# Kernel tuning notes

Measured on AMD Instinct MI355X. Metric: run time of the kernel, lower is better.

Reference implementation:

```python
import jax, jax.numpy as jnp
import numpy as np

NUM_REL = 20000
NUM_EDGES = 640000
DIM_IN = 128
DIM_OUT = 128
NUM_HEAD = 8
DIM_HID = DIM_OUT // NUM_HEAD
NUM_BIN = 10
NEG_SLOPE = 0.2


def leaky_relu(x):
    return jnp.where(x >= 0, x, NEG_SLOPE * x)


def setup_inputs() -> dict:
    key = jax.random.key(0)
    ks = jax.random.split(key, 8)
    emb_rel = jax.random.normal(ks[0], (NUM_REL, DIM_IN), dtype=jnp.float32)
    head = jax.random.randint(ks[1], (NUM_EDGES, 1), 0, NUM_REL)
    tail = jax.random.randint(ks[2], (NUM_EDGES, 1), 0, NUM_REL)
    bins = jax.random.randint(ks[3], (NUM_EDGES, 1), 0, NUM_BIN)
    relation_triplets = jnp.concatenate([head, tail, bins], axis=-1).astype(jnp.int64)
    # xavier-normal-ish init
    attn_proj_w = jax.random.normal(ks[4], (DIM_OUT, 2 * DIM_IN), dtype=jnp.float32) * (2.0 / np.sqrt(2 * DIM_IN + DIM_OUT))
    attn_proj_b = jnp.zeros((DIM_OUT,), dtype=jnp.float32)
    attn_bin = jax.random.normal(ks[5], (NUM_BIN, NUM_HEAD, 1), dtype=jnp.float32) * 0.3
    attn_vec = jax.random.normal(ks[6], (1, NUM_HEAD, DIM_HID), dtype=jnp.float32) * (2.0 / np.sqrt(NUM_HEAD * DIM_HID))
    aggr_proj_w = jax.random.normal(ks[7], (DIM_OUT, DIM_IN), dtype=jnp.float32) * (2.0 / np.sqrt(DIM_IN + DIM_OUT))
    aggr_proj_b = jnp.zeros((DIM_OUT,), dtype=jnp.float32)
    return {"emb_rel": emb_rel, "relation_triplets": relation_triplets,
            "attn_proj_w": attn_proj_w, "attn_proj_b": attn_proj_b,
            "attn_bin": attn_bin, "attn_vec": attn_vec,
            "aggr_proj_w": aggr_proj_w, "aggr_proj_b": aggr_proj_b}


def reference(emb_rel, relation_triplets, attn_proj_w, attn_proj_b, attn_bin, attn_vec, aggr_proj_w, aggr_proj_b):
    num_rel = emb_rel.shape[0]
    head = relation_triplets[..., 0]
    tail = relation_triplets[..., 1]
    bins = relation_triplets[..., 2]
    # edge gather + concat: [E, 2*dim_in]
    concat = jnp.concatenate([emb_rel[head], emb_rel[tail]], axis=-1)
    proj = concat @ attn_proj_w.T + attn_proj_b  # [E, dim_out]
    proj = leaky_relu(proj).reshape(-1, NUM_HEAD, DIM_HID)
    attn_raw = (proj * attn_vec).sum(axis=-1, keepdims=True) + leaky_relu(attn_bin[bins])  # [E,H,1]
    # per-head-relation segment softmax over edges grouped by head index
    seg_max = jax.ops.segment_max(attn_raw, head, num_segments=num_rel)  # [R,H,1]
    attn_val = jnp.exp(attn_raw - seg_max[head])
    seg_sum = jax.ops.segment_sum(attn_val, head, num_segments=num_rel)  # [R,H,1]
    beta = attn_val / (seg_sum[head] + 1e-16)
    msg = (emb_rel[tail] @ aggr_proj_w.T + aggr_proj_b).reshape(-1, NUM_HEAD, DIM_HID)
    out = jax.ops.segment_sum(beta * msg, head, num_segments=num_rel)  # [R,H,Dh]
    return out.reshape(num_rel, -1)
```

## Files before the change

### kernel.cpp

```cpp
#include <hip/hip_runtime.h>
#include <hip/hip_bf16.h>
#include <cstdint>
#include <cstddef>

#define NUM_REL    20000
#define NUM_EDGES  640000
#define DIM        128
#define NUM_HEAD   8
#define DIM_HID    16
#define NUM_BIN    10
#define CAP        128
#define PROJ_BLKS  471
#define SC_BLKS    2500

using u16 = unsigned short;
using u32 = unsigned int;
typedef __attribute__((ext_vector_type(8))) short bf16x8;
typedef __attribute__((ext_vector_type(4))) float f32x4;

__device__ __forceinline__ float b2f(u16 u) { return __uint_as_float(((u32)u) << 16); }
__device__ __forceinline__ float lo2f(u32 u) { return __uint_as_float(u << 16); }
__device__ __forceinline__ float hi2f(u32 u) { return __uint_as_float(u & 0xffff0000u); }
__device__ __forceinline__ float lrelu(float x) { return fmaxf(x, 0.2f * x); }
__device__ __forceinline__ int clampi(int v, int hi) { return v < 0 ? 0 : (v > hi ? hi : v); }
__device__ __forceinline__ float ldf(const void* p, int f32m, int i)
{ return f32m ? ((const float*)p)[i] : b2f(((const u16*)p)[i]); }
__device__ __forceinline__ u16 f2b(float x)
{ u32 u = __float_as_uint(x); u += 0x7fffu + ((u >> 16) & 1u); return (u16)(u >> 16); }
__device__ __forceinline__ u32 pk2(float a, float b)
{ return (u32)f2b(a) | ((u32)f2b(b) << 16); }

__global__ __launch_bounds__(256) void k_detect(
    const int* __restrict__ trip, const u16* __restrict__ emb,
    int* __restrict__ flags, int* __restrict__ cnt)
{
    int idx = blockIdx.x * 256 + threadIdx.x;
    if (idx < NUM_REL) cnt[idx] = 0;
    if (blockIdx.x == 0 && threadIdx.x < 64) {
        int t = threadIdx.x;
        bool odd_zero = (trip[2 * t + 1] == 0) && (trip[2 * t + 129] == 0);
        unsigned long long m1 = __ballot(odd_zero);
        int e = (emb[2 * t] >> 7) & 0xFF;
        bool inr = (e >= 110) && (e <= 136);
        unsigned long long m2 = __ballot(inr);
        if (t == 0) {
            flags[0] = (~m1 == 0ull) ? 1 : 0;
            flags[1] = (__popcll(m2) >= 32) ? 0 : 1;
        }
    }
}

__global__ __launch_bounds__(256) void k_projscatter(
    const void* __restrict__ emb, const int* __restrict__ trip,
    const void* __restrict__ w_attn, const void* __restrict__ w_aggr,
    const void* __restrict__ b_attn, const void* __restrict__ b_aggr,
    const int* __restrict__ flags,
    float* __restrict__ A, u16* __restrict__ Bb, u16* __restrict__ Mb,
    int* __restrict__ cnt, int* __restrict__ bucket)
{
    __shared__ u16 sA[128 * 128];
    __shared__ u16 sW[128 * 128];
    __shared__ float sBias[128];

    const int f32m = flags[1];
    const int tid = threadIdx.x;

    if (blockIdx.x >= PROJ_BLKS) {
        int e = (blockIdx.x - PROJ_BLKS) * 256 + tid;
        if (e < NUM_EDGES) {
            int h, t, b;
            if (flags[0]) { h = trip[6 * e]; t = trip[6 * e + 2]; b = trip[6 * e + 4]; }
            else          { h = trip[3 * e]; t = trip[3 * e + 1]; b = trip[3 * e + 2]; }
            h = clampi(h, NUM_REL - 1);
            t = clampi(t, NUM_REL - 1);
            b = clampi(b, NUM_BIN - 1);
            int pos = atomicAdd(&cnt[h], 1);
            if (pos < CAP) bucket[h * CAP + pos] = t | (b << 20);
        }
        return;
    }

    const int mt = blockIdx.x / 3, nt = blockIdx.x % 3;
    const int r0 = mt * 128;

    if (tid < 128)
        sBias[tid] = (nt == 0) ? 0.f : ldf((nt == 1) ? b_attn : b_aggr, f32m, tid);

    if (f32m) {
        const float* src = (const float*)emb;
        #pragma unroll
        for (int i = 0; i < 16; ++i) {
            int f = i * 256 + tid;
            int row = f >> 5, pos = f & 31;
            int g = r0 + row;
            float4 x = (g < NUM_REL) ? ((const float4*)(src + (size_t)g * DIM))[pos]
                                     : make_float4(0.f, 0.f, 0.f, 0.f);
            int chunk = (pos >> 1) ^ (row & 15);
            *(uint2*)&sA[row * 128 + chunk * 8 + (pos & 1) * 4] =
                make_uint2(pk2(x.x, x.y), pk2(x.z, x.w));
        }
    } else {
        const u16* src = (const u16*)emb;
        #pragma unroll
        for (int i = 0; i < 8; ++i) {
            int f = i * 256 + tid;
            int row = f >> 4, pos = f & 15;
            int g = r0 + row;
            uint4 x = (g < NUM_REL) ? ((const uint4*)(src + (size_t)g * DIM))[pos]
                                    : make_uint4(0, 0, 0, 0);
            int chunk = pos ^ (row & 15);
            *(uint4*)&sA[row * 128 + chunk * 8] = x;
        }
    }

    {
        const void* wsrc = (nt == 2) ? w_aggr : w_attn;
        const int stride = (nt == 2) ? 128 : 256;
        const int koff   = (nt == 1) ? 128 : 0;
        if (f32m) {
            const float* src = (const float*)wsrc;
            #pragma unroll
            for (int i = 0; i < 16; ++i) {
                int f = i * 256 + tid;
                int row = f >> 5, pos = f & 31;
                float4 x = ((const float4*)(src + (size_t)row * stride + koff))[pos];
                int chunk = (pos >> 1) ^ (row & 15);
                *(uint2*)&sW[row * 128 + chunk * 8 + (pos & 1) * 4] =
                    make_uint2(pk2(x.x, x.y), pk2(x.z, x.w));
            }
        } else {
            const u16* src = (const u16*)wsrc;
            #pragma unroll
            for (int i = 0; i < 8; ++i) {
                int f = i * 256 + tid;
                int row = f >> 4, pos = f & 15;
                uint4 x = ((const uint4*)(src + (size_t)row * stride + koff))[pos];
                int chunk = pos ^ (row & 15);
                *(uint4*)&sW[row * 128 + chunk * 8] = x;
            }
        }
    }
    __syncthreads();

    const int lane = tid & 63, wid = tid >> 6;
    const int wm = (wid >> 1) * 64, wn = (wid & 1) * 64;
    const int ln15 = lane & 15, q = lane >> 4;

    f32x4 acc[4][4] = {};
    #pragma unroll
    for (int kk = 0; kk < 4; ++kk) {
        const int cbase = kk * 4 + q;
        bf16x8 a[4], b[4];
        #pragma unroll
        for (int mi = 0; mi < 4; ++mi) {
            int m = wm + mi * 16 + ln15;
            int c = cbase ^ ln15;
            a[mi] = *(const bf16x8*)&sA[m * 128 + c * 8];
        }
        #pragma unroll
        for (int ni = 0; ni < 4; ++ni) {
            int n = wn + ni * 16 + ln15;
            int c = cbase ^ ln15;
            b[ni] = *(const bf16x8*)&sW[n * 128 + c * 8];
        }
        #pragma unroll
        for (int mi = 0; mi < 4; ++mi)
            #pragma unroll
            for (int ni = 0; ni < 4; ++ni)
                acc[mi][ni] = __builtin_amdgcn_mfma_f32_16x16x32_bf16(
                    a[mi], b[ni], acc[mi][ni], 0, 0, 0);
    }

    #pragma unroll
    for (int mi = 0; mi < 4; ++mi) {
        #pragma unroll
        for (int reg = 0; reg < 4; ++reg) {
            int g = r0 + wm + mi * 16 + q * 4 + reg;
            if (g < NUM_REL) {
                #pragma unroll
                for (int ni = 0; ni < 4; ++ni) {
                    int c = wn + ni * 16 + ln15;
                    float v = acc[mi][ni][reg] + sBias[c];
                    size_t o = (size_t)g * DIM + c;
                    if (nt == 0)      A[o]  = v;
                    else if (nt == 1) Bb[o] = f2b(v);
                    else              Mb[o] = f2b(v);
                }
            }
        }
    }
}

__global__ __launch_bounds__(256, 6) void k_segment(
    const float* __restrict__ A, const u16* __restrict__ Bb,
    const u16* __restrict__ Mb, const void* __restrict__ attn_bin,
    const void* __restrict__ attn_vec, const int* __restrict__ cnt,
    const int* __restrict__ bucket, const int* __restrict__ flags,
    void* __restrict__ out)
{
    __shared__ float sAr[4][DIM];
    __shared__ float sVec[DIM];
    __shared__ float sBin[NUM_BIN * NUM_HEAD];

    const int f32m = flags[1];
    const int tid  = threadIdx.x;
    const int wid  = tid >> 6, lane = tid & 63;
    const int r = blockIdx.x * 4 + wid;
    int nE = cnt[r]; if (nE > CAP) nE = CAP;
    const int* __restrict__ bk = bucket + r * CAP;

    {
        const float2* ap = (const float2*)(A + (size_t)r * DIM);
        float2 a2 = ap[lane];
        sAr[wid][2 * lane] = a2.x; sAr[wid][2 * lane + 1] = a2.y;
    }
    if (tid < DIM) sVec[tid] = ldf(attn_vec, f32m, tid);
    else if (tid < DIM + NUM_BIN * NUM_HEAD)
        sBin[tid - DIM] = lrelu(ldf(attn_bin, f32m, tid - DIM));
    __syncthreads();

    if (nE == 0) {
        if (f32m) ((float2*)out)[(size_t)r * 64 + lane] = make_float2(0.f, 0.f);
        else      ((u32*)out)[(size_t)r * 64 + lane] = 0;
        return;
    }

    const int el = lane >> 3, hd = lane & 7;
    const int ah = lane >> 3;

    float av[16], vv[16];
    {
        const float4* pA = (const float4*)(&sAr[wid][hd * DIM_HID]);
        const float4* pV = (const float4*)(&sVec[hd * DIM_HID]);
        #pragma unroll
        for (int i = 0; i < 4; ++i) {
            float4 a4 = pA[i], v4 = pV[i];
            av[4*i+0]=a4.x; av[4*i+1]=a4.y; av[4*i+2]=a4.z; av[4*i+3]=a4.w;
            vv[4*i+0]=v4.x; vv[4*i+1]=v4.y; vv[4*i+2]=v4.z; vv[4*i+3]=v4.w;
        }
    }

    float l = 0.f, accx = 0.f, accy = 0.f;

    for (int base = 0; base < nE; base += 8) {
        int e = base + el;
        bool act = e < nE;
        int tb = 0;
        if (act) tb = bk[e];
        int t = tb & 0xFFFFF;
        float p = 0.f;
        if (act) {
            int b = (tb >> 20) & 0xF;
            const uint4* Bt = (const uint4*)(Bb + (size_t)t * DIM) + hd * 2;
            uint4 q0 = Bt[0], q1 = Bt[1];
            float s = sBin[b * NUM_HEAD + hd];
            s += lrelu(av[0]  + lo2f(q0.x)) * vv[0];
            s += lrelu(av[1]  + hi2f(q0.x)) * vv[1];
            s += lrelu(av[2]  + lo2f(q0.y)) * vv[2];
            s += lrelu(av[3]  + hi2f(q0.y)) * vv[3];
            s += lrelu(av[4]  + lo2f(q0.z)) * vv[4];
            s += lrelu(av[5]  + hi2f(q0.z)) * vv[5];
            s += lrelu(av[6]  + lo2f(q0.w)) * vv[6];
            s += lrelu(av[7]  + hi2f(q0.w)) * vv[7];
            s += lrelu(av[8]  + lo2f(q1.x)) * vv[8];
            s += lrelu(av[9]  + hi2f(q1.x)) * vv[9];
            s += lrelu(av[10] + lo2f(q1.y)) * vv[10];
            s += lrelu(av[11] + hi2f(q1.y)) * vv[11];
            s += lrelu(av[12] + lo2f(q1.z)) * vv[12];
            s += lrelu(av[13] + hi2f(q1.z)) * vv[13];
            s += lrelu(av[14] + lo2f(q1.w)) * vv[14];
            s += lrelu(av[15] + hi2f(q1.w)) * vv[15];
            s = fminf(fmaxf(s, -60.f), 60.f);
            p = __expf(s);
        }
        l += p;

        int lim = nE - base; if (lim > 8) lim = 8;
        #pragma unroll
        for (int k = 0; k < 8; ++k) {
            if (k < lim) {
                float v = __shfl(p, k * 8 + ah);
                int tk  = __shfl(t, k * 8);
                u32 mm = *(const u32*)(Mb + (size_t)tk * DIM + 2 * lane);
                accx += v * lo2f(mm);
                accy += v * hi2f(mm);
            }
        }
    }

    float lt = l + __shfl_xor(l, 8);
    lt += __shfl_xor(lt, 16);
    lt += __shfl_xor(lt, 32);
    float lA = __shfl(lt, ah);
    float inv = 1.0f / (lA + 1e-16f);
    float o0 = accx * inv, o1 = accy * inv;
    if (f32m) {
        ((float2*)out)[(size_t)r * 64 + lane] = make_float2(o0, o1);
    } else {
        u32 pk = (u32)f2b(o0) | ((u32)f2b(o1) << 16);
        ((u32*)out)[(size_t)r * 64 + lane] = pk;
    }
}

extern "C" void kernel_launch(void* const* d_in, const int* in_sizes, int n_in,
                              void* d_out, int out_size, void* d_ws, size_t ws_size,
                              hipStream_t stream)
{
    (void)in_sizes; (void)n_in; (void)out_size; (void)ws_size;
    const void* emb      = d_in[0];
    const int*  trip     = (const int*)d_in[1];
    const void* w_attn   = d_in[2];
    const void* b_attn   = d_in[3];
    const void* attn_bin = d_in[4];
    const void* attn_vec = d_in[5];
    const void* w_aggr   = d_in[6];
    const void* b_aggr   = d_in[7];

    char* p = (char*)d_ws;
    float* A      = (float*)p; p += (size_t)NUM_REL * DIM * 4;
    u16*   Bb     = (u16*)p;   p += (size_t)NUM_REL * DIM * 2;
    u16*   Mb     = (u16*)p;   p += (size_t)NUM_REL * DIM * 2;
    int*   bucket = (int*)p;   p += (size_t)NUM_REL * CAP * 4;
    int*   cnt    = (int*)p;   p += (size_t)NUM_REL * 4;
    int*   flags  = (int*)p;   p += 256;

    k_detect<<<80, 256, 0, stream>>>(trip, (const u16*)emb, flags, cnt);
    k_projscatter<<<PROJ_BLKS + SC_BLKS, 256, 0, stream>>>(
        emb, trip, w_attn, w_aggr, b_attn, b_aggr, flags, A, Bb, Mb, cnt, bucket);
    k_segment<<<NUM_REL / 4, 256, 0, stream>>>(A, Bb, Mb, attn_bin, attn_vec,
                                               cnt, bucket, flags, d_out);
}
```

Measured before the change: 189.6 us.

## Inline format detection per block and software-prefetch next edge batch in segment loop

Removes the separate detect kernel: each block now recomputes the format flags in shared memory, and the count array is zeroed with a memset. In the segment kernel, the bucket entry and Bb row for the next group of 8 edges are loaded before computing the current group, so gather latency overlaps with compute. The cost is redundant flag detection in every block, an extra __syncthreads, higher register pressure from the prefetched values, and always-issued loads for inactive edges (these fall back to row 0).

```diff
diff --git a/kernel.cpp b/kernel.cpp
--- a/kernel.cpp
+++ b/kernel.cpp
@@ -30,47 +30,46 @@
 __device__ __forceinline__ u32 pk2(float a, float b)
 { return (u32)f2b(a) | ((u32)f2b(b) << 16); }
 
-__global__ __launch_bounds__(256) void k_detect(
-    const int* __restrict__ trip, const u16* __restrict__ emb,
-    int* __restrict__ flags, int* __restrict__ cnt)
+__device__ __forceinline__ void detect_flags(const int* __restrict__ trip,
+                                             const u16* __restrict__ emb,
+                                             int* sF, int tid)
 {
-    int idx = blockIdx.x * 256 + threadIdx.x;
-    if (idx < NUM_REL) cnt[idx] = 0;
-    if (blockIdx.x == 0 && threadIdx.x < 64) {
-        int t = threadIdx.x;
-        bool odd_zero = (trip[2 * t + 1] == 0) && (trip[2 * t + 129] == 0);
+    if (tid < 64) {
+        bool odd_zero = (trip[2 * tid + 1] == 0) && (trip[2 * tid + 129] == 0);
         unsigned long long m1 = __ballot(odd_zero);
-        int e = (emb[2 * t] >> 7) & 0xFF;
-        bool inr = (e >= 110) && (e <= 136);
+        int ex = (emb[2 * tid] >> 7) & 0xFF;
+        bool inr = (ex >= 110) && (ex <= 136);
         unsigned long long m2 = __ballot(inr);
-        if (t == 0) {
-            flags[0] = (~m1 == 0ull) ? 1 : 0;
-            flags[1] = (__popcll(m2) >= 32) ? 0 : 1;
-        }
-    }
+        if (tid == 0) {
+            sF[0] = (~m1 == 0ull) ? 1 : 0;
+            sF[1] = (__popcll(m2) >= 32) ? 0 : 1;
+        }
+    }
+    __syncthreads();
 }
 
 __global__ __launch_bounds__(256) void k_projscatter(
     const void* __restrict__ emb, const int* __restrict__ trip,
     const void* __restrict__ w_attn, const void* __restrict__ w_aggr,
     const void* __restrict__ b_attn, const void* __restrict__ b_aggr,
-    const int* __restrict__ flags,
     float* __restrict__ A, u16* __restrict__ Bb, u16* __restrict__ Mb,
     int* __restrict__ cnt, int* __restrict__ bucket)
 {
     __shared__ u16 sA[128 * 128];
     __shared__ u16 sW[128 * 128];
     __shared__ float sBias[128];
-
-    const int f32m = flags[1];
+    __shared__ int sF[2];
+
     const int tid = threadIdx.x;
+    detect_flags(trip, (const u16*)emb, sF, tid);
+    const int is64 = sF[0], f32m = sF[1];
 
     if (blockIdx.x >= PROJ_BLKS) {
         int e = (blockIdx.x - PROJ_BLKS) * 256 + tid;
         if (e < NUM_EDGES) {
             int h, t, b;
-            if (flags[0]) { h = trip[6 * e]; t = trip[6 * e + 2]; b = trip[6 * e + 4]; }
-            else          { h = trip[3 * e]; t = trip[3 * e + 1]; b = trip[3 * e + 2]; }
+            if (is64) { h = trip[6 * e]; t = trip[6 * e + 2]; b = trip[6 * e + 4]; }
+            else      { h = trip[3 * e]; t = trip[3 * e + 1]; b = trip[3 * e + 2]; }
             h = clampi(h, NUM_REL - 1);
             t = clampi(t, NUM_REL - 1);
             b = clampi(b, NUM_BIN - 1);
@@ -195,15 +194,18 @@
     const float* __restrict__ A, const u16* __restrict__ Bb,
     const u16* __restrict__ Mb, const void* __restrict__ attn_bin,
     const void* __restrict__ attn_vec, const int* __restrict__ cnt,
-    const int* __restrict__ bucket, const int* __restrict__ flags,
-    void* __restrict__ out)
+    const int* __restrict__ bucket, const int* __restrict__ trip,
+    const void* __restrict__ emb, void* __restrict__ out)
 {
     __shared__ float sAr[4][DIM];
     __shared__ float sVec[DIM];
     __shared__ float sBin[NUM_BIN * NUM_HEAD];
-
-    const int f32m = flags[1];
+    __shared__ int sF[2];
+
     const int tid  = threadIdx.x;
+    detect_flags(trip, (const u16*)emb, sF, tid);
+    const int f32m = sF[1];
+
     const int wid  = tid >> 6, lane = tid & 63;
     const int r = blockIdx.x * 4 + wid;
     int nE = cnt[r]; if (nE > CAP) nE = CAP;
@@ -242,17 +244,23 @@
 
     float l = 0.f, accx = 0.f, accy = 0.f;
 
+    bool act = el < nE;
+    int tb = act ? bk[el] : 0;
+    int t  = tb & 0xFFFFF;
+    const uint4* Bt0p = (const uint4*)(Bb + (size_t)t * DIM) + hd * 2;
+    uint4 q0 = Bt0p[0], q1 = Bt0p[1];
+
     for (int base = 0; base < nE; base += 8) {
-        int e = base + el;
-        bool act = e < nE;
-        int tb = 0;
-        if (act) tb = bk[e];
-        int t = tb & 0xFFFFF;
+        int e_n = base + 8 + el;
+        bool act_n = e_n < nE;
+        int tb_n = act_n ? bk[e_n] : 0;
+        int t_n  = tb_n & 0xFFFFF;
+        const uint4* Btn = (const uint4*)(Bb + (size_t)t_n * DIM) + hd * 2;
+        uint4 q0n = Btn[0], q1n = Btn[1];
+
         float p = 0.f;
-        if (act) {
+        {
             int b = (tb >> 20) & 0xF;
-            const uint4* Bt = (const uint4*)(Bb + (size_t)t * DIM) + hd * 2;
-            uint4 q0 = Bt[0], q1 = Bt[1];
             float s = sBin[b * NUM_HEAD + hd];
             s += lrelu(av[0]  + lo2f(q0.x)) * vv[0];
             s += lrelu(av[1]  + hi2f(q0.x)) * vv[1];
@@ -271,7 +279,7 @@
             s += lrelu(av[14] + lo2f(q1.w)) * vv[14];
             s += lrelu(av[15] + hi2f(q1.w)) * vv[15];
             s = fminf(fmaxf(s, -60.f), 60.f);
-            p = __expf(s);
+            p = act ? __expf(s) : 0.f;
         }
         l += p;
 
@@ -286,6 +294,8 @@
                 accy += v * hi2f(mm);
             }
         }
+
+        act = act_n; tb = tb_n; t = t_n; q0 = q0n; q1 = q1n;
     }
 
     float lt = l + __shfl_xor(l, 8);
@@ -322,11 +332,10 @@
     u16*   Mb     = (u16*)p;   p += (size_t)NUM_REL * DIM * 2;
     int*   bucket = (int*)p;   p += (size_t)NUM_REL * CAP * 4;
     int*   cnt    = (int*)p;   p += (size_t)NUM_REL * 4;
-    int*   flags  = (int*)p;   p += 256;
-
-    k_detect<<<80, 256, 0, stream>>>(trip, (const u16*)emb, flags, cnt);
+
+    hipMemsetAsync(cnt, 0, NUM_REL * sizeof(int), stream);
     k_projscatter<<<PROJ_BLKS + SC_BLKS, 256, 0, stream>>>(
-        emb, trip, w_attn, w_aggr, b_attn, b_aggr, flags, A, Bb, Mb, cnt, bucket);
+        emb, trip, w_attn, w_aggr, b_attn, b_aggr, A, Bb, Mb, cnt, bucket);
     k_segment<<<NUM_REL / 4, 256, 0, stream>>>(A, Bb, Mb, attn_bin, attn_vec,
-                                               cnt, bucket, flags, d_out);
+                                               cnt, bucket, trip, emb, d_out);
 }
```

Result: slower. 194.7 us (+2.7%).
